# Performance work log

Measured on AMD Instinct MI355X. Metric: run time of the kernel, lower is better.

Reference implementation:

```python
import jax, jax.numpy as jnp
import numpy as np

P_ITER = 30   # Krylov iterations (p_iter=30 in source)
N_PROBE = 100 # stochastic probe vectors (t=100 in source)


def setup_inputs() -> dict:
    N, t, r = 8192, N_PROBE, 256
    key = jax.random.key(0)
    kA, ky, kz = jax.random.split(key, 3)
    # Well-conditioned SPD kernel + noise matrix: K = A A^T / r + I
    A = jax.random.normal(kA, (N, r), dtype=jnp.float32)
    Knn_noise = (A @ A.T) / r + jnp.eye(N, dtype=jnp.float32)
    y = jax.random.normal(ky, (N, 1), dtype=jnp.float32)
    # Rademacher probes (||z||^2 = N exactly)
    Z = jnp.where(jax.random.normal(kz, (N, t)) >= 0, 1.0, -1.0).astype(jnp.float32)
    return {"Knn_noise": Knn_noise, "y": y, "Z": Z}


def _batched_cg(K, B, p_iter):
    """Batched conjugate gradients on K X = B, tracking Lanczos coefficients.
    B: [N, M]. Returns X [N, M], alphas [p, M], betas [p, M]."""
    X = jnp.zeros_like(B)
    R = B
    P = B
    rs = jnp.sum(R * R, axis=0)  # [M]

    def step(carry, _):
        X, R, P, rs = carry
        V = K @ P                               # [N, M] dense matvec (GEMM)
        pv = jnp.sum(P * V, axis=0)             # [M]
        alpha = rs / pv
        X = X + alpha * P
        R = R - alpha * V
        rs_new = jnp.sum(R * R, axis=0)
        beta = rs_new / rs
        P = R + beta * P
        return (X, R, P, rs_new), (alpha, beta)

    (X, _, _, _), (alphas, betas) = jax.lax.scan(step, (X, R, P, rs), None, length=p_iter)
    return X, alphas, betas


def _slq_logdet(alphas, betas, N):
    """Stochastic Lanczos quadrature logdet from CG coefficients.
    alphas, betas: [p, t] (one column per probe)."""
    inv_a = 1.0 / alphas                                   # [p, t]
    diag = inv_a.at[1:].add(betas[:-1] / alphas[:-1])      # T diagonal  [p, t]
    off = jnp.sqrt(betas[:-1]) / alphas[:-1]               # T off-diag  [p-1, t]

    def make_T(d, o):
        return jnp.diag(d) + jnp.diag(o, 1) + jnp.diag(o, -1)

    Ts = jax.vmap(make_T, in_axes=(1, 1))(diag, off)       # [t, p, p]
    lam, V = jnp.linalg.eigh(Ts)                           # small p x p eig per probe
    lam = jnp.maximum(lam, 1e-12)
    # z^T log(K) z ~= ||z||^2 * e1^T Vexp log(Lam) V^T e1 ; ||z||^2 = N (Rademacher)
    quad = jnp.sum(V[:, 0, :] ** 2 * jnp.log(lam), axis=1)  # [t]
    return N * jnp.mean(quad)


def reference(Knn_noise, y, Z):
    N = y.shape[0]
    B = jnp.concatenate([y, Z], axis=1)                    # solve + probes together
    X, alphas, betas = _batched_cg(Knn_noise, B, P_ITER)
    Knn_i_y = X[:, :1]                                     # K^{-1} y
    log_det = _slq_logdet(alphas[:, 1:], betas[:, 1:], N)  # SLQ logdet from probes
    two_pi = jnp.asarray(2.0 * np.pi, dtype=y.dtype)
    return -0.5 * (y.T @ Knn_i_y) - 0.5 * log_det - N * 0.5 * jnp.log(two_pi)
```

## Files before the change

### kernel.cpp

```cpp
#include <hip/hip_runtime.h>
#include <hip/hip_fp16.h>

#define NN 8192
#define NCOLS 101
#define CPW 112
#define BN 128
#define BM 128
#define KSPL 8
#define KCH (NN / KSPL)
#define NSTEP (KCH / 128)
#define PITER 30
#define PVLD 104

typedef __attribute__((ext_vector_type(4))) float f32x4;

__device__ __forceinline__ void async_copy16(const void* g, void* l) {
  __builtin_amdgcn_global_load_lds(
      (const __attribute__((address_space(1))) unsigned int*)g,
      (__attribute__((address_space(3))) unsigned int*)l, 16, 0, 0);
}

__device__ __forceinline__ unsigned int pack_fp8x4(float x, float y, float z, float w) {
  unsigned int v = __builtin_amdgcn_cvt_pk_fp8_f32(x, y, 0, false);
  v = __builtin_amdgcn_cvt_pk_fp8_f32(z, w, v, true);
  return v;
}

__device__ __forceinline__ float block_sum(float v) {
  #pragma unroll
  for (int o = 32; o > 0; o >>= 1) v += __shfl_down(v, o);
  __shared__ float sw[4];
  int w = threadIdx.x >> 6;
  if ((threadIdx.x & 63) == 0) sw[w] = v;
  __syncthreads();
  float r = 0.f;
  if (threadIdx.x < 4) r = sw[threadIdx.x];
  r += __shfl_down(r, 2);
  r += __shfl_down(r, 1);
  return r;
}

__global__ __launch_bounds__(256, 2) void gemm_kernel(
    const unsigned char* __restrict__ Kb,
    const unsigned char* __restrict__ Pb,
    const float* __restrict__ Pf,
    const float* __restrict__ SCit,
    __half* __restrict__ Vp,
    float* __restrict__ pvp) {
  __shared__ __align__(16) unsigned char smem[65536];
  unsigned char* sA = smem;
  unsigned char* sB = smem + 32768;
  float* sC = (float*)smem;

  int bx = blockIdx.x;
  int kz = bx & 7;
  int rb = bx >> 3;
  int tid = threadIdx.x;
  int lane = tid & 63;
  int w = tid >> 6;
  int r0 = rb * BM;
  int k0 = kz * KCH;
  int lrow = lane >> 3;
  int gseg = (lane & 7) ^ lrow;
  int mm = lane & 15;
  int quad = lane >> 4;
  int q1 = quad >> 1, q0 = quad & 1;
  int wm = w >> 1, wn = w & 1;

  int aBase[4], aXor[4], bBase[4], bXor[4];
  #pragma unroll
  for (int i = 0; i < 4; ++i) {
    int arow = wm * 64 + i * 16 + mm;
    aBase[i] = arow * 128 + (q0 << 3);
    aXor[i] = (arow & 7) << 4;
    int bcol = wn * 64 + i * 16 + mm;
    bBase[i] = bcol * 128 + (q0 << 3);
    bXor[i] = (bcol & 7) << 4;
  }

  f32x4 acc[4][4];
  #pragma unroll
  for (int i = 0; i < 4; ++i)
    #pragma unroll
    for (int j = 0; j < 4; ++j) acc[i][j] = (f32x4){0.f, 0.f, 0.f, 0.f};

  auto stage = [&](int s, int buf) {
    int kk = k0 + s * 128;
    #pragma unroll
    for (int q = 0; q < 4; ++q) {
      async_copy16(Kb + (size_t)(r0 + w * 32 + q * 8 + lrow) * NN + kk + gseg * 16,
                   sA + buf * 16384 + (w * 32 + q * 8) * 128);
      async_copy16(Pb + (size_t)(w * 32 + q * 8 + lrow) * NN + kk + gseg * 16,
                   sB + buf * 16384 + (w * 32 + q * 8) * 128);
    }
  };

  stage(0, 0);
  __syncthreads();

  #pragma unroll 2
  for (int s = 0; s < NSTEP; ++s) {
    int cur = s & 1;
    if (s + 1 < NSTEP) stage(s + 1, cur ^ 1);
    const unsigned char* A = sA + cur * 16384;
    const unsigned char* B = sB + cur * 16384;
    #pragma unroll
    for (int kh = 0; kh < 4; ++kh) {
      int s16 = (kh * 2 + q1) << 4;
      long long aF[4], bF[4];
      #pragma unroll
      for (int i = 0; i < 4; ++i) {
        aF[i] = *(const long long*)(A + aBase[i] + (s16 ^ aXor[i]));
        bF[i] = *(const long long*)(B + bBase[i] + (s16 ^ bXor[i]));
      }
      #pragma unroll
      for (int i = 0; i < 4; ++i)
        #pragma unroll
        for (int j = 0; j < 4; ++j)
          acc[i][j] = __builtin_amdgcn_mfma_f32_16x16x32_fp8_fp8(aF[i], bF[j], acc[i][j], 0, 0, 0);
    }
    __syncthreads();
  }
  #pragma unroll
  for (int i = 0; i < 4; ++i)
    #pragma unroll
    for (int j = 0; j < 4; ++j) {
      int ctile = wn * 64 + j * 16;
      if (ctile >= CPW) continue;
      #pragma unroll
      for (int r = 0; r < 4; ++r)
        sC[(wm * 64 + i * 16 + quad * 4 + r) * 113 + ctile + mm] = acc[i][j][r];
    }
  __syncthreads();
  const size_t SPL = (size_t)CPW * NN;
  __half* Vout = Vp + (size_t)kz * SPL;
  for (int idx = tid; idx < BM * CPW; idx += 256) {
    int col = idx >> 7;
    int row = idx & 127;
    if (col < NCOLS)
      Vout[(size_t)col * NN + r0 + row] = __float2half(sC[row * 113 + col] * SCit[col]);
  }
  int rr = tid & 63;
  int g = tid >> 6;
  for (int j = 0; j < 26; ++j) {
    int c = g + j * 4;
    float prod = 0.f;
    if (c < NCOLS)
      prod = (sC[rr * 113 + c] * Pf[(size_t)c * NN + r0 + rr] +
              sC[(rr + 64) * 113 + c] * Pf[(size_t)c * NN + r0 + 64 + rr]) * SCit[c];
    #pragma unroll
    for (int o = 32; o > 0; o >>= 1) prod += __shfl_down(prod, o);
    if (rr == 0 && c < NCOLS) pvp[(size_t)bx * PVLD + c] = prod;
  }
}

__global__ void update1_kernel(const __half* __restrict__ Vp,
                               const float* __restrict__ Pf,
                               float* __restrict__ R,
                               float* __restrict__ X0,
                               const float* __restrict__ pvp,
                               const float* __restrict__ rs,
                               float* __restrict__ rs_new,
                               float* __restrict__ alphas) {
  const size_t SPL = (size_t)CPW * NN;
  __shared__ float s_alpha;
  int c = blockIdx.y;
  int t = threadIdx.x;
  float pvv = pvp[(size_t)t * PVLD + c] + pvp[(size_t)(t + 256) * PVLD + c];
  float pvtot = block_sum(pvv);
  if (t == 0) s_alpha = rs[c] / pvtot;
  __syncthreads();
  float alpha = s_alpha;

  size_t off = (size_t)c * NN + blockIdx.x * 1024 + t * 4;
  float4 v = {0.f, 0.f, 0.f, 0.f};
  #pragma unroll
  for (int sp = 0; sp < KSPL; ++sp) {
    const __half2* p = (const __half2*)(Vp + sp * SPL + off);
    float2 f01 = __half22float2(p[0]);
    float2 f23 = __half22float2(p[1]);
    v.x += f01.x; v.y += f01.y; v.z += f23.x; v.w += f23.y;
  }
  float4 r = *(float4*)(R + off);
  r.x -= alpha * v.x; r.y -= alpha * v.y; r.z -= alpha * v.z; r.w -= alpha * v.w;
  *(float4*)(R + off) = r;
  if (c == 0) {
    size_t xo = blockIdx.x * 1024 + t * 4;
    float4 x = *(float4*)(X0 + xo);
    float4 p = *(const float4*)(Pf + off);
    x.x += alpha * p.x; x.y += alpha * p.y; x.z += alpha * p.z; x.w += alpha * p.w;
    *(float4*)(X0 + xo) = x;
  }
  float rn = r.x * r.x + r.y * r.y + r.z * r.z + r.w * r.w;
  float tot = block_sum(rn);
  if (t == 0) {
    atomicAdd(rs_new + c, tot);
    if (blockIdx.x == 0) alphas[c] = alpha;
  }
}

__global__ void update2_kernel(const float* __restrict__ R,
                               float* __restrict__ P,
                               unsigned char* __restrict__ Pb,
                               const float* __restrict__ rs,
                               const float* __restrict__ rs_new,
                               const float* __restrict__ PNold,
                               float* __restrict__ PNnew,
                               float* __restrict__ SCnew,
                               float* __restrict__ betas) {
  int c = blockIdx.y;
  float rsn = rs_new[c];
  float beta = rsn / rs[c];
  float pnn = rsn + beta * beta * PNold[c];
  float sc = exp2f(roundf(0.5f * log2f(pnn * (1.f / 8192.f))));
  float inv = 1.f / sc;
  size_t off = (size_t)c * NN + blockIdx.x * 1024 + threadIdx.x * 4;
  float4 r = *(const float4*)(R + off);
  float4 p = *(float4*)(P + off);
  p.x = r.x + beta * p.x; p.y = r.y + beta * p.y;
  p.z = r.z + beta * p.z; p.w = r.w + beta * p.w;
  *(float4*)(P + off) = p;
  *(unsigned int*)(Pb + off) = pack_fp8x4(p.x * inv, p.y * inv, p.z * inv, p.w * inv);
  if (threadIdx.x == 0 && blockIdx.x == 0) {
    betas[c] = beta;
    PNnew[c] = pnn;
    SCnew[c] = sc;
  }
}

__global__ void cast_k_kernel(const float* __restrict__ K, unsigned char* __restrict__ Kb) {
  size_t i = ((size_t)blockIdx.x * 256 + threadIdx.x) * 4;
  size_t stride = (size_t)gridDim.x * 1024;
  for (; i < (size_t)NN * NN; i += stride) {
    float4 f = *(const float4*)(K + i);
    *(unsigned int*)(Kb + i) = pack_fp8x4(f.x, f.y, f.z, f.w);
  }
}

__global__ void init_vec_kernel(const float* __restrict__ y, const float* __restrict__ Z,
                                float* __restrict__ P, float* __restrict__ R,
                                unsigned char* __restrict__ Pb) {
  int c = blockIdx.y;
  int i = blockIdx.x * 256 + threadIdx.x;
  float val = (c == 0) ? y[i] : Z[(size_t)i * 100 + (c - 1)];
  size_t off = (size_t)c * NN + i;
  P[off] = val;
  R[off] = val;
  Pb[off] = (unsigned char)(__builtin_amdgcn_cvt_pk_fp8_f32(val, 0.f, 0, false) & 0xFF);
}

#define NSMALL 23424
__global__ void init_misc_kernel(float* __restrict__ X0, float* __restrict__ smalls,
                                 unsigned char* __restrict__ Pbpad) {
  const int total = 8192 + NSMALL + 27 * NN;
  for (int t = blockIdx.x * 256 + threadIdx.x; t < total; t += gridDim.x * 256) {
    if (t < 8192) X0[t] = 0.f;
    else if (t < 8192 + NSMALL) smalls[t - 8192] = 0.f;
    else Pbpad[t - (8192 + NSMALL)] = 0;
  }
}

__global__ void init_rs_kernel(const float* __restrict__ y, float* __restrict__ rs0,
                               float* __restrict__ pn0, float* __restrict__ sc0) {
  int t = threadIdx.x;
  float s = 0.f;
  for (int i = t; i < NN; i += 256) { float v = y[i]; s += v * v; }
  float tot = block_sum(s);
  if (t == 0) { rs0[0] = tot; pn0[0] = tot; }
  if (t >= 1 && t <= 100) { rs0[t] = (float)NN; pn0[t] = (float)NN; }
  if (t < 128) sc0[t] = 1.f;
}

__global__ __launch_bounds__(64, 1) void slq_kernel(
    const float* __restrict__ AL, const float* __restrict__ BE,
    float* __restrict__ QP) {
  __shared__ double sd[PITER], se[PITER];
  int lane = threadIdx.x;
  int c = blockIdx.x + 1;
  if (lane < PITER) {
    double a = (double)AL[lane * 128 + c];
    double dd = 1.0 / a;
    if (lane > 0) {
      double ap = (double)AL[(lane - 1) * 128 + c];
      double bp = (double)BE[(lane - 1) * 128 + c];
      dd += bp / ap;
    }
    sd[lane] = dd;
    double ee = 0.0;
    if (lane < PITER - 1) {
      double b = (double)BE[lane * 128 + c];
      ee = sqrt(b) / a;
    }
    se[lane] = ee;
  }
  __syncthreads();
  double d[PITER], e[PITER];
  #pragma unroll
  for (int i = 0; i < PITER; ++i) { d[i] = sd[i]; e[i] = se[i]; }

  float quadk = 0.f;
  if (lane < PITER) {
    double lo = 1e300, hi = -1e300;
    #pragma unroll
    for (int i = 0; i < PITER; ++i) {
      double r = e[i] + (i > 0 ? e[i - 1] : 0.0);
      lo = fmin(lo, d[i] - r);
      hi = fmax(hi, d[i] + r);
    }
    int k = lane;
    for (int it = 0; it < 48; ++it) {
      double mid = 0.5 * (lo + hi);
      int cnt = 0;
      double q = d[0] - mid;
      cnt += (q < 0.0);
      #pragma unroll
      for (int i = 1; i < PITER; ++i) {
        double aq = fabs(q);
        if (aq < 1e-30) q = (q < 0.0) ? -1e-30 : 1e-30;
        q = d[i] - mid - (e[i - 1] * e[i - 1]) / q;
        cnt += (q < 0.0);
      }
      if (cnt > k) hi = mid; else lo = mid;
    }
    double lam = 0.5 * (lo + hi);
    double e0 = fmax(e[0], 1e-150);
    double vprev = 1.0;
    double vcur = (lam - d[0]) / e0;
    double s = 1.0 + vcur * vcur;
    double scale2 = 1.0;
    #pragma unroll
    for (int i = 1; i < PITER - 1; ++i) {
      double ei = fmax(e[i], 1e-150);
      double vnext = ((lam - d[i]) * vcur - e[i - 1] * vprev) / ei;
      if (fabs(vnext) > 1e150) {
        vnext *= 1e-150; vcur *= 1e-150; s *= 1e-300; scale2 *= 1e-300;
      }
      vprev = vcur; vcur = vnext;
      s += vcur * vcur;
    }
    double w = scale2 / s;
    double lc = lam > 1e-12 ? lam : 1e-12;
    quadk = (float)(w * log(lc));
  }
  #pragma unroll
  for (int o = 32; o > 0; o >>= 1) quadk += __shfl_down(quadk, o);
  if (lane == 0) QP[blockIdx.x] = quadk;
}

__global__ void final2_kernel(const float* __restrict__ y, const float* __restrict__ X0,
                              const float* __restrict__ QP, float* __restrict__ out) {
  int t = threadIdx.x;
  float s = 0.f;
  for (int i = t; i < NN; i += 256) s += y[i] * X0[i];
  float ydot = block_sum(s);
  __syncthreads();
  float q = (t < 100) ? QP[t] : 0.f;
  float qsum = block_sum(q);
  if (t == 0) {
    float logdet = (float)NN * (qsum * 0.01f);
    out[0] = -0.5f * ydot - 0.5f * logdet - (float)NN * 0.5f * 1.8378770664093454f;
  }
}

extern "C" void kernel_launch(void* const* d_in, const int* in_sizes, int n_in,
                              void* d_out, int out_size, void* d_ws, size_t ws_size,
                              hipStream_t stream) {
  const float* K = (const float*)d_in[0];
  const float* y = (const float*)d_in[1];
  const float* Z = (const float*)d_in[2];
  float* out = (float*)d_out;
  char* ws = (char*)d_ws;
  if (ws_size < 89796096ull) return;

  unsigned char* Kb = (unsigned char*)(ws + 0ull);
  unsigned char* Pb = (unsigned char*)(ws + 67108864ull);
  float* P   = (float*)(ws + 68157440ull);
  float* R   = (float*)(ws + 71467008ull);
  __half* Vp = (__half*)(ws + 74776576ull);
  float* X0  = (float*)(ws + 89456640ull);
  float* PVP = (float*)(ws + 89489408ull);
  float* SM  = (float*)(ws + 89702400ull);
  float* RS = SM;
  float* AL = SM + 7808;
  float* BE = SM + 11648;
  float* PN = SM + 15488;
  float* SC = SM + 19456;
  float* QP = (float*)(ws + 74776576ull);

  cast_k_kernel<<<8192, 256, 0, stream>>>(K, Kb);
  init_vec_kernel<<<dim3(32, 101), 256, 0, stream>>>(y, Z, P, R, Pb);
  init_misc_kernel<<<240, 256, 0, stream>>>(X0, SM, Pb + (size_t)NCOLS * NN);
  init_rs_kernel<<<1, 256, 0, stream>>>(y, RS, PN, SC);

  for (int it = 0; it < PITER; ++it) {
    gemm_kernel<<<512, 256, 0, stream>>>(Kb, Pb, P, SC + it * 128, Vp, PVP);
    update1_kernel<<<dim3(8, 101), 256, 0, stream>>>(Vp, P, R, X0, PVP,
        RS + it * 128, RS + (it + 1) * 128, AL + it * 128);
    update2_kernel<<<dim3(8, 101), 256, 0, stream>>>(R, P, Pb, RS + it * 128,
        RS + (it + 1) * 128, PN + it * 128, PN + (it + 1) * 128,
        SC + (it + 1) * 128, BE + it * 128);
  }
  slq_kernel<<<100, 64, 0, stream>>>(AL, BE, QP);
  final2_kernel<<<1, 256, 0, stream>>>(y, X0, QP, out);
}
```

Before: 1.989 ms.

## Fuse the whole CG loop into one cooperative persistent kernel with grid syncs

Replaces the cast, init and 30 iterations of gemm/update1/update2 launches with a single cooperative kernel of 512 blocks that uses grid.sync between phases. This is meant to remove about 94 kernel launches and their launch gaps. It falls back to the old multi-kernel path if the cooperative launch fails. The risk is grid-sync overhead and the need for all 512 blocks at 256 threads with 64KB LDS to be co-resident (2 per CU). If they cannot be, the launch fails and the fallback path runs instead.

```diff
diff --git a/kernel.cpp b/kernel.cpp
--- a/kernel.cpp
+++ b/kernel.cpp
@@ -1,5 +1,8 @@
 #include <hip/hip_runtime.h>
 #include <hip/hip_fp16.h>
+#include <hip/hip_cooperative_groups.h>
+
+namespace cg = cooperative_groups;
 
 #define NN 8192
 #define NCOLS 101
@@ -11,6 +14,7 @@
 #define NSTEP (KCH / 128)
 #define PITER 30
 #define PVLD 104
+#define NSMALL 23424
 
 typedef __attribute__((ext_vector_type(4))) float f32x4;
 
@@ -27,9 +31,10 @@
 }
 
 __device__ __forceinline__ float block_sum(float v) {
+  __shared__ float sw[4];
+  __syncthreads();
   #pragma unroll
   for (int o = 32; o > 0; o >>= 1) v += __shfl_down(v, o);
-  __shared__ float sw[4];
   int w = threadIdx.x >> 6;
   if ((threadIdx.x & 63) == 0) sw[w] = v;
   __syncthreads();
@@ -38,6 +43,236 @@
   r += __shfl_down(r, 2);
   r += __shfl_down(r, 1);
   return r;
+}
+
+__global__ __launch_bounds__(256, 2) void cg_fused(
+    const float* __restrict__ K, const float* __restrict__ y,
+    const float* __restrict__ Z, unsigned char* __restrict__ Kb,
+    unsigned char* __restrict__ Pb, float* __restrict__ P,
+    float* __restrict__ R, __half* __restrict__ Vp, float* __restrict__ X0,
+    float* __restrict__ pvp, float* __restrict__ SM) {
+  cg::grid_group grid = cg::this_grid();
+  __shared__ __align__(16) unsigned char smem[65536];
+  unsigned char* sA = smem;
+  unsigned char* sB = smem + 32768;
+  float* sC = (float*)smem;
+  __shared__ float s_alpha;
+
+  float* RS = SM;
+  float* rsp = SM + 3968;
+  float* AL = SM + 7808;
+  float* BE = SM + 11648;
+  float* PN = SM + 15488;
+  float* SC = SM + 19456;
+
+  int b = blockIdx.x;
+  int t = threadIdx.x;
+  int lane = t & 63;
+  int w = t >> 6;
+
+  for (size_t i = ((size_t)b * 256 + t) * 4; i < (size_t)NN * NN; i += (size_t)512 * 1024) {
+    float4 f = *(const float4*)(K + i);
+    *(unsigned int*)(Kb + i) = pack_fp8x4(f.x, f.y, f.z, f.w);
+  }
+  for (int v = b; v < 3232; v += 512) {
+    int xi = v & 31, c = v >> 5;
+    int i = xi * 256 + t;
+    float val = (c == 0) ? y[i] : Z[(size_t)i * 100 + (c - 1)];
+    size_t off = (size_t)c * NN + i;
+    P[off] = val;
+    R[off] = val;
+    Pb[off] = (unsigned char)(__builtin_amdgcn_cvt_pk_fp8_f32(val, 0.f, 0, false) & 0xFF);
+  }
+  {
+    const int total = 8192 + NSMALL + 27 * NN;
+    for (int i = b * 256 + t; i < total; i += 512 * 256) {
+      if (i < 8192) X0[i] = 0.f;
+      else if (i < 8192 + NSMALL) SM[i - 8192] = 0.f;
+      else Pb[(size_t)NCOLS * NN + (i - (8192 + NSMALL))] = 0;
+    }
+  }
+  grid.sync();
+  if (b == 0) {
+    float s = 0.f;
+    for (int i = t; i < NN; i += 256) { float vv = y[i]; s += vv * vv; }
+    float tot = block_sum(s);
+    if (t == 0) { RS[0] = tot; PN[0] = tot; }
+    if (t >= 1 && t <= 100) { RS[t] = (float)NN; PN[t] = (float)NN; }
+    if (t < 128) SC[t] = 1.f;
+  }
+  grid.sync();
+
+  int kz = b & 7;
+  int rb = b >> 3;
+  int r0 = rb * BM;
+  int k0 = kz * KCH;
+  int lrow = lane >> 3;
+  int gseg = (lane & 7) ^ lrow;
+  int mm = lane & 15;
+  int quad = lane >> 4;
+  int q1 = quad >> 1, q0 = quad & 1;
+  int wm = w >> 1, wn = w & 1;
+  int aBase[4], aXor[4], bBase[4], bXor[4];
+  #pragma unroll
+  for (int i = 0; i < 4; ++i) {
+    int arow = wm * 64 + i * 16 + mm;
+    aBase[i] = arow * 128 + (q0 << 3);
+    aXor[i] = (arow & 7) << 4;
+    int bcol = wn * 64 + i * 16 + mm;
+    bBase[i] = bcol * 128 + (q0 << 3);
+    bXor[i] = (bcol & 7) << 4;
+  }
+  const size_t SPL = (size_t)CPW * NN;
+  int vx = b & 7;
+  int vc1 = b >> 3;
+  bool has2 = (b < 296);
+  int vc2 = 64 + (b >> 3);
+
+  for (int it = 0; it < PITER; ++it) {
+    const float* SCit = SC + (size_t)it * 128;
+    f32x4 acc[4][4];
+    #pragma unroll
+    for (int i = 0; i < 4; ++i)
+      #pragma unroll
+      for (int j = 0; j < 4; ++j) acc[i][j] = (f32x4){0.f, 0.f, 0.f, 0.f};
+
+    auto stage = [&](int s, int buf) {
+      int kk = k0 + s * 128;
+      #pragma unroll
+      for (int q = 0; q < 4; ++q) {
+        async_copy16(Kb + (size_t)(r0 + w * 32 + q * 8 + lrow) * NN + kk + gseg * 16,
+                     sA + buf * 16384 + (w * 32 + q * 8) * 128);
+        async_copy16(Pb + (size_t)(w * 32 + q * 8 + lrow) * NN + kk + gseg * 16,
+                     sB + buf * 16384 + (w * 32 + q * 8) * 128);
+      }
+    };
+
+    stage(0, 0);
+    __syncthreads();
+
+    #pragma unroll 2
+    for (int s = 0; s < NSTEP; ++s) {
+      int cur = s & 1;
+      if (s + 1 < NSTEP) stage(s + 1, cur ^ 1);
+      const unsigned char* A = sA + cur * 16384;
+      const unsigned char* B = sB + cur * 16384;
+      #pragma unroll
+      for (int kh = 0; kh < 4; ++kh) {
+        int s16 = (kh * 2 + q1) << 4;
+        long long aF[4], bF[4];
+        #pragma unroll
+        for (int i = 0; i < 4; ++i) {
+          aF[i] = *(const long long*)(A + aBase[i] + (s16 ^ aXor[i]));
+          bF[i] = *(const long long*)(B + bBase[i] + (s16 ^ bXor[i]));
+        }
+        #pragma unroll
+        for (int i = 0; i < 4; ++i)
+          #pragma unroll
+          for (int j = 0; j < 4; ++j)
+            acc[i][j] = __builtin_amdgcn_mfma_f32_16x16x32_fp8_fp8(aF[i], bF[j], acc[i][j], 0, 0, 0);
+      }
+      __syncthreads();
+    }
+    #pragma unroll
+    for (int i = 0; i < 4; ++i)
+      #pragma unroll
+      for (int j = 0; j < 4; ++j) {
+        int ctile = wn * 64 + j * 16;
+        if (ctile >= CPW) continue;
+        #pragma unroll
+        for (int r = 0; r < 4; ++r)
+          sC[(wm * 64 + i * 16 + quad * 4 + r) * 113 + ctile + mm] = acc[i][j][r];
+      }
+    __syncthreads();
+    {
+      __half* Vout = Vp + (size_t)kz * SPL;
+      for (int idx = t; idx < BM * CPW; idx += 256) {
+        int col = idx >> 7;
+        int row = idx & 127;
+        if (col < NCOLS)
+          Vout[(size_t)col * NN + r0 + row] = __float2half(sC[row * 113 + col] * SCit[col]);
+      }
+      int rr = t & 63;
+      int g = t >> 6;
+      for (int j = 0; j < 26; ++j) {
+        int c = g + j * 4;
+        float prod = 0.f;
+        if (c < NCOLS)
+          prod = (sC[rr * 113 + c] * P[(size_t)c * NN + r0 + rr] +
+                  sC[(rr + 64) * 113 + c] * P[(size_t)c * NN + r0 + 64 + rr]) * SCit[c];
+        #pragma unroll
+        for (int o = 32; o > 0; o >>= 1) prod += __shfl_down(prod, o);
+        if (rr == 0 && c < NCOLS) pvp[(size_t)b * PVLD + c] = prod;
+      }
+    }
+    grid.sync();
+
+    for (int rep = 0; rep < 2; ++rep) {
+      if (rep == 1 && !has2) break;
+      int c = (rep == 0) ? vc1 : vc2;
+      float pvv = pvp[(size_t)t * PVLD + c] + pvp[(size_t)(t + 256) * PVLD + c];
+      float pvtot = block_sum(pvv);
+      if (t == 0) s_alpha = RS[(size_t)it * 128 + c] / pvtot;
+      __syncthreads();
+      float alpha = s_alpha;
+      size_t off = (size_t)c * NN + vx * 1024 + t * 4;
+      float4 vsum = {0.f, 0.f, 0.f, 0.f};
+      #pragma unroll
+      for (int sp = 0; sp < KSPL; ++sp) {
+        const __half2* ph = (const __half2*)(Vp + sp * SPL + off);
+        float2 f01 = __half22float2(ph[0]);
+        float2 f23 = __half22float2(ph[1]);
+        vsum.x += f01.x; vsum.y += f01.y; vsum.z += f23.x; vsum.w += f23.y;
+      }
+      float4 r = *(float4*)(R + off);
+      r.x -= alpha * vsum.x; r.y -= alpha * vsum.y;
+      r.z -= alpha * vsum.z; r.w -= alpha * vsum.w;
+      *(float4*)(R + off) = r;
+      if (c == 0) {
+        size_t xo = (size_t)vx * 1024 + t * 4;
+        float4 x = *(float4*)(X0 + xo);
+        float4 p = *(const float4*)(P + off);
+        x.x += alpha * p.x; x.y += alpha * p.y;
+        x.z += alpha * p.z; x.w += alpha * p.w;
+        *(float4*)(X0 + xo) = x;
+      }
+      float rn = r.x * r.x + r.y * r.y + r.z * r.z + r.w * r.w;
+      float tot = block_sum(rn);
+      if (t == 0) {
+        rsp[vx * 128 + c] = tot;
+        if (vx == 0) AL[(size_t)it * 128 + c] = alpha;
+      }
+    }
+    grid.sync();
+
+    for (int rep = 0; rep < 2; ++rep) {
+      if (rep == 1 && !has2) break;
+      int c = (rep == 0) ? vc1 : vc2;
+      float rsn = 0.f;
+      #pragma unroll
+      for (int xx = 0; xx < 8; ++xx) rsn += rsp[xx * 128 + c];
+      float beta = rsn / RS[(size_t)it * 128 + c];
+      if (it < PITER - 1) {
+        float pnn = rsn + beta * beta * PN[(size_t)it * 128 + c];
+        float sc = exp2f(roundf(0.5f * log2f(pnn * (1.f / 8192.f))));
+        float inv = 1.f / sc;
+        size_t off = (size_t)c * NN + vx * 1024 + t * 4;
+        float4 r = *(const float4*)(R + off);
+        float4 p = *(float4*)(P + off);
+        p.x = r.x + beta * p.x; p.y = r.y + beta * p.y;
+        p.z = r.z + beta * p.z; p.w = r.w + beta * p.w;
+        *(float4*)(P + off) = p;
+        *(unsigned int*)(Pb + off) = pack_fp8x4(p.x * inv, p.y * inv, p.z * inv, p.w * inv);
+        if (vx == 0 && t == 0) {
+          PN[(size_t)(it + 1) * 128 + c] = pnn;
+          SC[(size_t)(it + 1) * 128 + c] = sc;
+          RS[(size_t)(it + 1) * 128 + c] = rsn;
+        }
+      }
+      if (vx == 0 && t == 0) BE[(size_t)it * 128 + c] = beta;
+    }
+    grid.sync();
+  }
 }
 
 __global__ __launch_bounds__(256, 2) void gemm_kernel(
@@ -249,7 +484,6 @@
   Pb[off] = (unsigned char)(__builtin_amdgcn_cvt_pk_fp8_f32(val, 0.f, 0, false) & 0xFF);
 }
 
-#define NSMALL 23424
 __global__ void init_misc_kernel(float* __restrict__ X0, float* __restrict__ smalls,
                                  unsigned char* __restrict__ Pbpad) {
   const int total = 8192 + NSMALL + 27 * NN;
@@ -288,8 +522,8 @@
     sd[lane] = dd;
     double ee = 0.0;
     if (lane < PITER - 1) {
-      double b = (double)BE[lane * 128 + c];
-      ee = sqrt(b) / a;
+      double bq = (double)BE[lane * 128 + c];
+      ee = sqrt(bq) / a;
     }
     se[lane] = ee;
   }
@@ -387,18 +621,24 @@
   float* SC = SM + 19456;
   float* QP = (float*)(ws + 74776576ull);
 
-  cast_k_kernel<<<8192, 256, 0, stream>>>(K, Kb);
-  init_vec_kernel<<<dim3(32, 101), 256, 0, stream>>>(y, Z, P, R, Pb);
-  init_misc_kernel<<<240, 256, 0, stream>>>(X0, SM, Pb + (size_t)NCOLS * NN);
-  init_rs_kernel<<<1, 256, 0, stream>>>(y, RS, PN, SC);
-
-  for (int it = 0; it < PITER; ++it) {
-    gemm_kernel<<<512, 256, 0, stream>>>(Kb, Pb, P, SC + it * 128, Vp, PVP);
-    update1_kernel<<<dim3(8, 101), 256, 0, stream>>>(Vp, P, R, X0, PVP,
-        RS + it * 128, RS + (it + 1) * 128, AL + it * 128);
-    update2_kernel<<<dim3(8, 101), 256, 0, stream>>>(R, P, Pb, RS + it * 128,
-        RS + (it + 1) * 128, PN + it * 128, PN + (it + 1) * 128,
-        SC + (it + 1) * 128, BE + it * 128);
+  void* args[] = {(void*)&K, (void*)&y, (void*)&Z, (void*)&Kb, (void*)&Pb,
+                  (void*)&P, (void*)&R, (void*)&Vp, (void*)&X0, (void*)&PVP,
+                  (void*)&SM};
+  hipError_t err = hipLaunchCooperativeKernel((const void*)cg_fused, dim3(512),
+                                              dim3(256), args, 0, stream);
+  if (err != hipSuccess) {
+    cast_k_kernel<<<8192, 256, 0, stream>>>(K, Kb);
+    init_vec_kernel<<<dim3(32, 101), 256, 0, stream>>>(y, Z, P, R, Pb);
+    init_misc_kernel<<<240, 256, 0, stream>>>(X0, SM, Pb + (size_t)NCOLS * NN);
+    init_rs_kernel<<<1, 256, 0, stream>>>(y, RS, PN, SC);
+    for (int it = 0; it < PITER; ++it) {
+      gemm_kernel<<<512, 256, 0, stream>>>(Kb, Pb, P, SC + it * 128, Vp, PVP);
+      update1_kernel<<<dim3(8, 101), 256, 0, stream>>>(Vp, P, R, X0, PVP,
+          RS + it * 128, RS + (it + 1) * 128, AL + it * 128);
+      update2_kernel<<<dim3(8, 101), 256, 0, stream>>>(R, P, Pb, RS + it * 128,
+          RS + (it + 1) * 128, PN + it * 128, PN + (it + 1) * 128,
+          SC + (it + 1) * 128, BE + it * 128);
+    }
   }
   slq_kernel<<<100, 64, 0, stream>>>(AL, BE, QP);
   final2_kernel<<<1, 256, 0, stream>>>(y, X0, QP, out);
```

Result: slower. 7.040 ms (+253.9%).
